# Kernel tuning notes

Hardware: AMD Instinct MI355X
Metric: run time of the kernel (lower is better)

## Reference

```python
import jax, jax.numpy as jnp
import numpy as np
from jax import lax

N, D, M, H = 8192, 32, 8, 128
ATOL = 1e-5
RTOL = 1e-5
MAX_STEPS = 10   # bounded adaptive dopri5 iterations (accept/reject with masking)
DT0 = 0.25


def setup_inputs() -> dict:
    key = jax.random.key(0)
    ks = jax.random.split(key, 6)
    p = lambda k, shape, s: jax.random.normal(k, shape, jnp.float32) * s
    return {
        "z": jax.random.normal(ks[0], (N, D), jnp.float32),
        "G_w": p(ks[1], (M, D), 0.3),
        "W1": p(ks[2], (H, D), (1.0 / D) ** 0.5),
        "b1": jnp.zeros((H,), jnp.float32),
        "W2": p(ks[3], (H, H), (1.0 / H) ** 0.5),
        "b2": jnp.zeros((H,), jnp.float32),
        "W3": p(ks[4], (D, H), (1.0 / H) ** 0.5),
        "b3": jnp.zeros((D,), jnp.float32),
        "T": jnp.ones((1,), jnp.float32),
    }


def qpnf_forward(z, G_w, W1, b1, W2, b2, W3, b3, T):
    d = z.shape[1]

    def mlp(x):  # dF network: d -> 128 -> 128 -> d
        h = jax.nn.relu(x @ W1.T + b1)
        h = jax.nn.relu(h @ W2.T + b2)
        return h @ W3.T + b3

    # G is linear (no bias) so jacrev(G)(x) == G_w for every sample; the batched
    # dG @ dG^T solves collapse to one shared (m,m) solve / (d,d) projector.
    A = G_w @ G_w.T                       # (m, m)
    AinvG = jnp.linalg.solve(A, G_w)      # (m, d) = A^{-1} W
    P = G_w.T @ AinvG                     # (d, d) null-space projector W^T A^{-1} W
    IP = jnp.eye(d, dtype=z.dtype) - P
    trP = jnp.trace(P)

    jac_mlp = jax.vmap(jax.jacrev(lambda xi: mlp(xi[None, :])[0]))  # (N,d,d)

    def f(y):  # augmented state y = [x | logp], dlogp/dt = -div(dx/dx)
        x = y[:, :d]
        dF = mlp(x)                        # (N, d)
        g = x @ G_w.T                      # (N, m)
        dz = -(dF @ IP) - g @ AinvG        # -(eta_J) - (eta_C)
        JdF = jac_mlp(x)                   # (N, d, d)
        # J_f = -(I-P) JdF - P  ->  dlogp = -trace(J_f)
        dlogp = jnp.einsum('jk,nkj->n', IP, JdF) + trP
        return jnp.concatenate([dz, dlogp[:, None]], axis=1)

    def rk_step(y, dt):  # Dormand-Prince 5(4)
        k1 = f(y)
        k2 = f(y + dt * (0.2 * k1))
        k3 = f(y + dt * (3/40 * k1 + 9/40 * k2))
        k4 = f(y + dt * (44/45 * k1 - 56/15 * k2 + 32/9 * k3))
        k5 = f(y + dt * (19372/6561 * k1 - 25360/2187 * k2 + 64448/6561 * k3 - 212/729 * k4))
        k6 = f(y + dt * (9017/3168 * k1 - 355/33 * k2 + 46732/5247 * k3 + 49/176 * k4 - 5103/18656 * k5))
        y1 = y + dt * (35/384 * k1 + 500/1113 * k3 + 125/192 * k4 - 2187/6784 * k5 + 11/84 * k6)
        k7 = f(y1)
        err = dt * ((35/384 - 5179/57600) * k1 + (500/1113 - 7571/16695) * k3
                    + (125/192 - 393/640) * k4 + (-2187/6784 + 92097/339200) * k5
                    + (11/84 - 187/2100) * k6 - (1/40) * k7)
        return y1, err

    t1 = 2.0 * T[0]  # eval path: integration_times[-1] *= 2
    y0 = jnp.concatenate([z, jnp.zeros((z.shape[0], 1), z.dtype)], axis=1)

    def body(carry, _):
        t, dt, y = carry
        done = t >= t1 - 1e-9
        dtc = jnp.where(done, jnp.asarray(1e-3, z.dtype), jnp.minimum(dt, t1 - t))
        y1, ev = rk_step(y, dtc)
        tol = ATOL + RTOL * jnp.maximum(jnp.abs(y), jnp.abs(y1))
        errn = jnp.sqrt(jnp.mean((ev / tol) ** 2))
        accept = jnp.logical_and(~done, errn <= 1.0)
        y_new = jnp.where(accept, y1, y)
        t_new = jnp.where(accept, t + dtc, t)
        factor = jnp.clip(0.9 * errn ** (-0.2), 0.2, 10.0)
        dt_new = jnp.where(done, dt, jnp.clip(dtc * factor, 1e-6, t1))
        dt_new = lax.stop_gradient(dt_new)
        return (t_new, dt_new, y_new), None

    init = (jnp.asarray(0.0, z.dtype), jnp.asarray(DT0, z.dtype), y0)
    (_, _, yT), _ = lax.scan(body, init, None, length=MAX_STEPS)
    return yT[:, :d]


def reference(z, G_w, W1, b1, W2, b2, W3, b3, T):
    return qpnf_forward(z, G_w, W1, b1, W2, b2, W3, b3, T)
```

## Files before the change

kernel.cpp:

```cpp
#include <hip/hip_runtime.h>
#include <hip/hip_cooperative_groups.h>
#include <math.h>

namespace cg = cooperative_groups;
typedef float4 f4;
typedef float2 f2;

#define NT 512
#define RB 32

#define WS_WR    0
#define WS_PART  32768
#define WS_TOTAL 35328

#define L_W1T   0
#define L_C3T   4096
#define L_PT    8320
#define L_XW    9472
#define L_H1W   10496
#define L_H2W   14592
#define L_KZ    18688
#define L_KL    26752
#define L_YZ    26976
#define L_Y1Z   28128
#define L_YL    29280
#define L_Y1L   29312
#define L_B1    29344
#define L_B2    29472
#define L_C0    29600
#define L_GS    29632
#define L_AAUG  29888
#define L_AINVG 30016
#define L_MISC  30272
#define LDS_FLOATS 30276
#define L_RED   L_H1W
#define L_P     L_H2W
#define L_IP    (L_H2W + 1024)
#define L_IPW3  L_KZ

__device__ const float ACO[5][5] = {
  { 0.2f, 0.f, 0.f, 0.f, 0.f },
  { (float)(3.0/40.0), (float)(9.0/40.0), 0.f, 0.f, 0.f },
  { (float)(44.0/45.0), (float)(-56.0/15.0), (float)(32.0/9.0), 0.f, 0.f },
  { (float)(19372.0/6561.0), (float)(-25360.0/2187.0), (float)(64448.0/6561.0), (float)(-212.0/729.0), 0.f },
  { (float)(9017.0/3168.0), (float)(-355.0/33.0), (float)(46732.0/5247.0), (float)(49.0/176.0), (float)(-5103.0/18656.0) }
};

#define B1C ((float)(35.0/384.0))
#define B3C ((float)(500.0/1113.0))
#define B4C ((float)(125.0/192.0))
#define B5C ((float)(-2187.0/6784.0))
#define B6C ((float)(11.0/84.0))

#define E1C ((float)(35.0/384.0 - 5179.0/57600.0))
#define E3C ((float)(500.0/1113.0 - 7571.0/16695.0))
#define E4C ((float)(125.0/192.0 - 393.0/640.0))
#define E5C ((float)(-2187.0/6784.0 + 92097.0/339200.0))
#define E6C ((float)(11.0/84.0 - 187.0/2100.0))
#define E7C ((float)(-1.0/40.0))

__device__ __forceinline__ f4 ld4(const float* p){ return *(const f4*)p; }
__device__ __forceinline__ void st4(float* p, f4 v){ *(f4*)p = v; }

__device__ __forceinline__ void assemble_x(float* lds, int tid, float dtc,
                                           const float* co, int np)
{
  const int w = tid >> 6, lane = tid & 63;
  const int r = lane >> 4;
  const int c = (lane << 1) & 31;
  const int o = (4 * w + r) * 36 + c;
  f2 y = *(const f2*)&lds[L_YZ + o];
  float sx = 0.f, sy = 0.f;
  for (int p = 0; p < np; p++){
    f2 kv = *(const f2*)&lds[L_KZ + p * 1152 + o];
    sx += co[p] * kv.x; sy += co[p] * kv.y;
  }
  float* XWp = &lds[L_XW + w * 128];
  XWp[(c + 0) * 4 + r] = y.x + dtc * sx;
  XWp[(c + 1) * 4 + r] = y.y + dtc * sy;
}

__device__ void eval_f(float* lds, const float* __restrict__ ws, int tid,
                       float trP, int kout)
{
  const int w = tid >> 6, lane = tid & 63;
  const int cg = lane & 31, kh = lane >> 5;
  float* XWp = &lds[L_XW  + w * 128];
  float* H1p = &lds[L_H1W + w * 512];
  float* H2p = &lds[L_H2W + w * 512];

  float a1[4][4];
#pragma unroll
  for (int i = 0; i < 4; i++)
#pragma unroll
    for (int j = 0; j < 4; j++) a1[i][j] = 0.f;
#pragma unroll 4
  for (int t = 0; t < 16; t++){
    const int k = kh * 16 + t;
    f4 xv = ld4(&XWp[k * 4]);
    f4 wv = ld4(&lds[L_W1T + k * 128 + 4 * cg]);
    const float* ap = (const float*)&xv;
    const float* bp = (const float*)&wv;
#pragma unroll
    for (int i = 0; i < 4; i++)
#pragma unroll
      for (int j = 0; j < 4; j++) a1[i][j] += bp[i] * ap[j];
  }
#pragma unroll
  for (int i = 0; i < 4; i++)
#pragma unroll
    for (int j = 0; j < 4; j++) a1[i][j] += __shfl_xor(a1[i][j], 32);
  if (kh == 0){
    f4 b1v = ld4(&lds[L_B1 + 4 * cg]);
    const float* b1p = (const float*)&b1v;
#pragma unroll
    for (int i = 0; i < 4; i++){
      f4 hv; float* hp = (float*)&hv;
#pragma unroll
      for (int j = 0; j < 4; j++) hp[j] = fmaxf(a1[i][j] + b1p[i], 0.f);
      st4(&H1p[(4 * cg + i) * 4], hv);
    }
  }
  __syncthreads();

  float ah[4][4], at[4][4];
#pragma unroll
  for (int i = 0; i < 4; i++)
#pragma unroll
    for (int j = 0; j < 4; j++){ ah[i][j] = 0.f; at[i][j] = 0.f; }
  const f4* WR4 = (const f4*)&ws[WS_WR];
  const int kb = kh * 64;
  f4 wb[4], rb[4];
#pragma unroll
  for (int u = 0; u < 4; u++){
    wb[u] = WR4[(kb + u) * 64 + cg];
    rb[u] = WR4[(kb + u) * 64 + 32 + cg];
  }
#pragma unroll 1
  for (int g = 0; g < 16; g++){
    f4 wc[4], rc[4];
#pragma unroll
    for (int u = 0; u < 4; u++){ wc[u] = wb[u]; rc[u] = rb[u]; }
    if (g < 15){
      const int kn = kb + (g + 1) * 4;
#pragma unroll
      for (int u = 0; u < 4; u++){
        wb[u] = WR4[(kn + u) * 64 + cg];
        rb[u] = WR4[(kn + u) * 64 + 32 + cg];
      }
    }
#pragma unroll
    for (int u = 0; u < 4; u++){
      const int k = kb + g * 4 + u;
      f4 av = ld4(&H1p[k * 4]);
      const float* ap = (const float*)&av;
      const float* wp = (const float*)&wc[u];
      const float* rp = (const float*)&rc[u];
      float m[4];
#pragma unroll
      for (int j = 0; j < 4; j++) m[j] = (ap[j] > 0.f) ? 1.f : 0.f;
#pragma unroll
      for (int i = 0; i < 4; i++)
#pragma unroll
        for (int j = 0; j < 4; j++){
          ah[i][j] += wp[i] * ap[j];
          at[i][j] += rp[i] * m[j];
        }
    }
  }
#pragma unroll
  for (int i = 0; i < 4; i++)
#pragma unroll
    for (int j = 0; j < 4; j++){
      ah[i][j] += __shfl_xor(ah[i][j], 32);
      at[i][j] += __shfl_xor(at[i][j], 32);
    }

  f4 b2v = ld4(&lds[L_B2 + 4 * cg]);
  const float* b2p = (const float*)&b2v;
  float h2v[4][4]; float dl[4] = {0.f, 0.f, 0.f, 0.f};
#pragma unroll
  for (int i = 0; i < 4; i++)
#pragma unroll
    for (int j = 0; j < 4; j++){
      float pre = ah[i][j] + b2p[i];
      float hv = fmaxf(pre, 0.f);
      h2v[i][j] = hv;
      if (pre > 0.f) dl[j] += at[i][j];
    }
#pragma unroll
  for (int mk = 1; mk < 32; mk <<= 1){
#pragma unroll
    for (int j = 0; j < 4; j++) dl[j] += __shfl_xor(dl[j], mk, 64);
  }
  if (kh == 0){
#pragma unroll
    for (int i = 0; i < 4; i++){
      f4 hv; float* hp = (float*)&hv;
#pragma unroll
      for (int j = 0; j < 4; j++) hp[j] = h2v[i][j];
      st4(&H2p[(4 * cg + i) * 4], hv);
    }
    if (cg == 0){
#pragma unroll
      for (int j = 0; j < 4; j++)
        lds[L_KL + kout * 32 + 4 * w + j] = dl[j] + trP;
    }
  }

  float a3[4] = {0.f, 0.f, 0.f, 0.f};
  const int bb = kh * 64;
#pragma unroll 4
  for (int t = 0; t < 16; t++){
    f4 cv = ld4(&lds[L_C3T + cg * 132 + bb + 4 * t]);
    const float* cp = (const float*)&cv;
#pragma unroll
    for (int u = 0; u < 4; u++){
      f4 av = ld4(&H2p[(bb + 4 * t + u) * 4]);
      const float* ap = (const float*)&av;
#pragma unroll
      for (int j = 0; j < 4; j++) a3[j] += ap[j] * cp[u];
    }
  }
  const int qq = kh * 16;
#pragma unroll
  for (int t = 0; t < 4; t++){
    f4 pv = ld4(&lds[L_PT + cg * 36 + qq + 4 * t]);
    const float* pp = (const float*)&pv;
#pragma unroll
    for (int u = 0; u < 4; u++){
      f4 av = ld4(&XWp[(qq + 4 * t + u) * 4]);
      const float* ap = (const float*)&av;
#pragma unroll
      for (int j = 0; j < 4; j++) a3[j] += ap[j] * pp[u];
    }
  }
#pragma unroll
  for (int j = 0; j < 4; j++) a3[j] += __shfl_xor(a3[j], 32);
  if (kh == 0){
    float c0v = lds[L_C0 + cg];
#pragma unroll
    for (int j = 0; j < 4; j++)
      lds[L_KZ + kout * 1152 + (4 * w + j) * 36 + cg] = -(a3[j] + c0v);
  }
}

__global__ void __launch_bounds__(NT, 2)
qpnf_kernel(const float* __restrict__ z, const float* __restrict__ Gw,
            const float* __restrict__ W1g, const float* __restrict__ b1g,
            const float* __restrict__ W2g, const float* __restrict__ b2g,
            const float* __restrict__ W3g, const float* __restrict__ b3g,
            const float* __restrict__ Tg, float* __restrict__ out,
            float* __restrict__ ws)
{
  __shared__ float lds[LDS_FLOATS];
  const int tid = threadIdx.x;
  const int bid = blockIdx.x;
  const int r0 = bid * RB;
  cg::grid_group grid = cg::this_grid();

  for (int i = 0; i < 8; i++){
    int idx = tid + i * NT;
    int h = idx >> 5, j = idx & 31;
    lds[L_W1T + j * 128 + h] = W1g[idx];
  }
  if (tid < 128){ lds[L_B1 + tid] = b1g[tid]; lds[L_B2 + tid] = b2g[tid]; }
  if (tid < 256) lds[L_GS + tid] = Gw[tid];
  __syncthreads();

  if (tid < 64){
    int i = tid >> 3, j = tid & 7;
    float s = 0.f;
    for (int k = 0; k < 32; k++) s += lds[L_GS + i * 32 + k] * lds[L_GS + j * 32 + k];
    lds[L_AAUG + i * 16 + j] = s;
    lds[L_AAUG + i * 16 + 8 + j] = (i == j) ? 1.f : 0.f;
  }
  __syncthreads();
  if (tid == 0){
    float* A = &lds[L_AAUG];
    for (int c = 0; c < 8; c++){
      int p = c; float mx = fabsf(A[c * 16 + c]);
      for (int r = c + 1; r < 8; r++){
        float v = fabsf(A[r * 16 + c]);
        if (v > mx){ mx = v; p = r; }
      }
      if (p != c)
        for (int q = 0; q < 16; q++){ float t = A[c*16+q]; A[c*16+q] = A[p*16+q]; A[p*16+q] = t; }
      float pv = 1.0f / A[c * 16 + c];
      for (int q = 0; q < 16; q++) A[c * 16 + q] *= pv;
      for (int r = 0; r < 8; r++) if (r != c){
        float fct = A[r * 16 + c];
        for (int q = 0; q < 16; q++) A[r * 16 + q] -= fct * A[c * 16 + q];
      }
    }
  }
  __syncthreads();
  if (tid < 256){
    int m = tid >> 5, d = tid & 31;
    float s = 0.f;
    for (int q = 0; q < 8; q++) s += lds[L_AAUG + m * 16 + 8 + q] * lds[L_GS + q * 32 + d];
    lds[L_AINVG + m * 32 + d] = s;
  }
  __syncthreads();
  for (int i4 = 0; i4 < 2; i4++){
    int idx = tid + i4 * NT;
    int i = idx >> 5, j = idx & 31;
    float s = 0.f;
    for (int m = 0; m < 8; m++) s += lds[L_GS + m * 32 + i] * lds[L_AINVG + m * 32 + j];
    lds[L_P + i * 32 + j] = s;
  }
  __syncthreads();
  float* IPl = &lds[L_IP];
  for (int i4 = 0; i4 < 2; i4++){
    int idx = tid + i4 * NT;
    int i = idx >> 5, j = idx & 31;
    IPl[i * 32 + j] = ((i == j) ? 1.f : 0.f) - lds[L_P + i * 32 + j];
  }
  if (tid == 0){
    float s = 0.f;
    for (int i = 0; i < 32; i++) s += lds[L_P + i * 32 + i];
    lds[L_MISC] = s;
  }
  __syncthreads();
  for (int i4 = 0; i4 < 8; i4++){
    int idx = tid + i4 * NT;
    int b = idx & 127, c = idx >> 7;
    float s = 0.f;
    for (int i = 0; i < 32; i++) s += W3g[i * 128 + b] * IPl[i * 32 + c];
    lds[L_C3T + c * 132 + b] = s;
  }
  for (int i4 = 0; i4 < 2; i4++){
    int idx = tid + i4 * NT;
    int c = idx >> 5, q = idx & 31;
    lds[L_PT + c * 36 + q] = lds[L_P + q * 32 + c];
  }
  if (tid < 32){
    float s = 0.f;
    for (int i = 0; i < 32; i++) s += b3g[i] * IPl[i * 32 + tid];
    lds[L_C0 + tid] = s;
  }
  for (int i4 = 0; i4 < 8; i4++){
    int idx = tid + i4 * NT;
    int j = idx >> 7, b = idx & 127;
    float s = 0.f;
    for (int k = 0; k < 32; k++) s += IPl[j * 32 + k] * W3g[k * 128 + b];
    lds[L_IPW3 + j * 128 + b] = s;
  }
  __syncthreads();
  if (bid < 128 && tid < 128){
    int a = bid;
    float s = 0.f;
    for (int j = 0; j < 32; j++) s += W1g[a * 32 + j] * lds[L_IPW3 + j * 128 + tid];
    ws[WS_WR + a * 256 + 128 + tid] = s * W2g[tid * 128 + a];
  }
  if (bid >= 128 && tid < 128){
    int a = bid - 128;
    ws[WS_WR + a * 256 + tid] = W2g[tid * 128 + a];
  }
  if (tid < 256){
    const int r = tid >> 3, jj = (tid & 7) * 4;
    st4(&lds[L_YZ + r * 36 + jj], ld4(&z[(r0 + r) * 32 + jj]));
  }
  if (tid < RB) lds[L_YL + tid] = 0.f;

  const float trP = lds[L_MISC];
  const float t1 = 2.0f * Tg[0];

  grid.sync();

  float t_cur = 0.f, dt_cur = 0.25f;
  bool prev_acc = false;

  for (int step = 0; step < 10; step++){
    if (t_cur >= t1 - 1e-9f) break;
    const float dtc = fminf(dt_cur, t1 - t_cur);

    for (int s = 1; s <= 6; s++){
      if (s == 1 && step > 0){
        if (prev_acc){
          const int w = tid >> 6, lane = tid & 63;
          const int r = lane >> 4, c = (lane << 1) & 31;
          const int o = (4 * w + r) * 36 + c;
          *(f2*)&lds[L_KZ + o] = *(const f2*)&lds[L_KZ + 6 * 1152 + o];
          if (lane < 4) lds[L_KL + 4 * w + lane] = lds[L_KL + 6 * 32 + 4 * w + lane];
        }
        continue;
      }
      assemble_x(lds, tid, dtc, ACO[s >= 2 ? s - 2 : 0], s - 1);
      eval_f(lds, ws, tid, trP, s - 1);
    }

    __syncthreads();
    if (tid < 256){
      const int r = tid >> 3, jj = (tid & 7) * 4;
      const int o = r * 36 + jj;
      f4 y   = ld4(&lds[L_YZ + o]);
      f4 k1v = ld4(&lds[L_KZ + 0 * 1152 + o]);
      f4 k3v = ld4(&lds[L_KZ + 2 * 1152 + o]);
      f4 k4v = ld4(&lds[L_KZ + 3 * 1152 + o]);
      f4 k5v = ld4(&lds[L_KZ + 4 * 1152 + o]);
      f4 k6v = ld4(&lds[L_KZ + 5 * 1152 + o]);
      f4 x;
      x.x = y.x + dtc * (B1C*k1v.x + B3C*k3v.x + B4C*k4v.x + B5C*k5v.x + B6C*k6v.x);
      x.y = y.y + dtc * (B1C*k1v.y + B3C*k3v.y + B4C*k4v.y + B5C*k5v.y + B6C*k6v.y);
      x.z = y.z + dtc * (B1C*k1v.z + B3C*k3v.z + B4C*k4v.z + B5C*k5v.z + B6C*k6v.z);
      x.w = y.w + dtc * (B1C*k1v.w + B3C*k3v.w + B4C*k4v.w + B5C*k5v.w + B6C*k6v.w);
      st4(&lds[L_Y1Z + o], x);
      float* XWp = &lds[L_XW + (r >> 2) * 128];
      const int rr = r & 3;
      XWp[(jj + 0) * 4 + rr] = x.x;
      XWp[(jj + 1) * 4 + rr] = x.y;
      XWp[(jj + 2) * 4 + rr] = x.z;
      XWp[(jj + 3) * 4 + rr] = x.w;
    }
    if (tid < RB){
      float s = B1C * lds[L_KL + 0*32 + tid] + B3C * lds[L_KL + 2*32 + tid]
              + B4C * lds[L_KL + 3*32 + tid] + B5C * lds[L_KL + 4*32 + tid]
              + B6C * lds[L_KL + 5*32 + tid];
      lds[L_Y1L + tid] = lds[L_YL + tid] + dtc * s;
    }
    __syncthreads();
    eval_f(lds, ws, tid, trP, 6);
    __syncthreads();

    float sacc = 0.f;
    if (tid < 256){
      const int r = tid >> 3, jj = (tid & 7) * 4;
      const int o = r * 36 + jj;
      f4 k1v = ld4(&lds[L_KZ + 0 * 1152 + o]);
      f4 k3v = ld4(&lds[L_KZ + 2 * 1152 + o]);
      f4 k4v = ld4(&lds[L_KZ + 3 * 1152 + o]);
      f4 k5v = ld4(&lds[L_KZ + 4 * 1152 + o]);
      f4 k6v = ld4(&lds[L_KZ + 5 * 1152 + o]);
      f4 k7v = ld4(&lds[L_KZ + 6 * 1152 + o]);
      f4 yv  = ld4(&lds[L_YZ + o]);
      f4 y1v = ld4(&lds[L_Y1Z + o]);
      float ev, tol, q;
      ev = dtc * (E1C*k1v.x + E3C*k3v.x + E4C*k4v.x + E5C*k5v.x + E6C*k6v.x + E7C*k7v.x);
      tol = 1e-5f + 1e-5f * fmaxf(fabsf(yv.x), fabsf(y1v.x)); q = ev / tol; sacc += q * q;
      ev = dtc * (E1C*k1v.y + E3C*k3v.y + E4C*k4v.y + E5C*k5v.y + E6C*k6v.y + E7C*k7v.y);
      tol = 1e-5f + 1e-5f * fmaxf(fabsf(yv.y), fabsf(y1v.y)); q = ev / tol; sacc += q * q;
      ev = dtc * (E1C*k1v.z + E3C*k3v.z + E4C*k4v.z + E5C*k5v.z + E6C*k6v.z + E7C*k7v.z);
      tol = 1e-5f + 1e-5f * fmaxf(fabsf(yv.z), fabsf(y1v.z)); q = ev / tol; sacc += q * q;
      ev = dtc * (E1C*k1v.w + E3C*k3v.w + E4C*k4v.w + E5C*k5v.w + E6C*k6v.w + E7C*k7v.w);
      tol = 1e-5f + 1e-5f * fmaxf(fabsf(yv.w), fabsf(y1v.w)); q = ev / tol; sacc += q * q;
    }
    if (tid < RB){
      float evl = dtc * (E1C * lds[L_KL + 0*32 + tid] + E3C * lds[L_KL + 2*32 + tid]
                + E4C * lds[L_KL + 3*32 + tid] + E5C * lds[L_KL + 4*32 + tid]
                + E6C * lds[L_KL + 5*32 + tid] + E7C * lds[L_KL + 6*32 + tid]);
      float toll = 1e-5f + 1e-5f * fmaxf(fabsf(lds[L_YL + tid]), fabsf(lds[L_Y1L + tid]));
      float ql = evl / toll; sacc += ql * ql;
    }
#pragma unroll
    for (int mk = 1; mk < 64; mk <<= 1) sacc += __shfl_xor(sacc, mk, 64);
    if ((tid & 63) == 0) lds[L_RED + (tid >> 6)] = sacc;
    __syncthreads();
    if (tid == 0){
      float s = lds[L_RED+0] + lds[L_RED+1] + lds[L_RED+2] + lds[L_RED+3]
              + lds[L_RED+4] + lds[L_RED+5] + lds[L_RED+6] + lds[L_RED+7];
      ws[WS_PART + step * 256 + bid] = s;
    }

    grid.sync();

    float ps = 0.f;
    if (tid < 256) ps = ws[WS_PART + step * 256 + tid];
#pragma unroll
    for (int mk = 1; mk < 64; mk <<= 1) ps += __shfl_xor(ps, mk, 64);
    if (tid < 256 && (tid & 63) == 0) lds[L_RED + (tid >> 6)] = ps;
    __syncthreads();
    const float errn = sqrtf((lds[L_RED+0] + lds[L_RED+1] + lds[L_RED+2] + lds[L_RED+3])
                             / 270336.0f);
    __syncthreads();

    const bool accept = (errn <= 1.0f);
    if (accept){
      const int w = tid >> 6, lane = tid & 63;
      const int r = lane >> 4, c = (lane << 1) & 31;
      const int o = (4 * w + r) * 36 + c;
      *(f2*)&lds[L_YZ + o] = *(const f2*)&lds[L_Y1Z + o];
      if (lane < 4) lds[L_YL + 4 * w + lane] = lds[L_Y1L + 4 * w + lane];
      t_cur += dtc;
    }
    float fac = 0.9f * powf(errn, -0.2f);
    fac = fminf(fmaxf(fac, 0.2f), 10.0f);
    dt_cur = fminf(fmaxf(dtc * fac, 1e-6f), t1);
    prev_acc = accept;
  }

  __syncthreads();
  if (tid < 256){
    const int r = tid >> 3, jj = (tid & 7) * 4;
    st4(&out[(r0 + r) * 32 + jj], ld4(&lds[L_YZ + r * 36 + jj]));
  }
}

extern "C" void kernel_launch(void* const* d_in, const int* in_sizes, int n_in,
                              void* d_out, int out_size, void* d_ws, size_t ws_size,
                              hipStream_t stream)
{
  (void)in_sizes; (void)n_in; (void)out_size;
  const float* z  = (const float*)d_in[0];
  const float* Gw = (const float*)d_in[1];
  const float* W1 = (const float*)d_in[2];
  const float* b1 = (const float*)d_in[3];
  const float* W2 = (const float*)d_in[4];
  const float* b2 = (const float*)d_in[5];
  const float* W3 = (const float*)d_in[6];
  const float* b3 = (const float*)d_in[7];
  const float* T  = (const float*)d_in[8];
  float* out = (float*)d_out;
  float* ws  = (float*)d_ws;
  if (ws_size < (size_t)WS_TOTAL * sizeof(float)) return;

  void* args[] = { (void*)&z, (void*)&Gw, (void*)&W1, (void*)&b1, (void*)&W2,
                   (void*)&b2, (void*)&W3, (void*)&b3, (void*)&T, (void*)&out,
                   (void*)&ws };
  hipLaunchCooperativeKernel((const void*)qpnf_kernel, dim3(256), dim3(NT),
                             args, 0, stream);
}
```

Baseline: 1.189 ms.

## Pair warps on two row groups in layer-2 GEMM to halve weight global loads

The layer-2 GEMM (h and Jacobian-trace accumulators) is restructured so each pair of wavefronts shares two 4-row groups and splits the K dimension, with each thread accumulating 8 columns instead of 4. Each wave now streams half as much of the W2/R weight data from global memory per row. Partial sums from the second wave go through a new LDS scratch area, which costs extra syncthreads and LDS. Launch bounds drop to one block per SM to allow the doubled accumulator register count, which reduces occupancy.

```diff
diff --git a/kernel.cpp b/kernel.cpp
--- a/kernel.cpp
+++ b/kernel.cpp
@@ -32,7 +32,8 @@
 #define L_AAUG  29888
 #define L_AINVG 30016
 #define L_MISC  30272
-#define LDS_FLOATS 30276
+#define L_S     30276
+#define LDS_FLOATS (30276 + 4*32*68)
 #define L_RED   L_H1W
 #define L_P     L_H2W
 #define L_IP    (L_H2W + 1024)
@@ -85,9 +86,22 @@
 {
   const int w = tid >> 6, lane = tid & 63;
   const int cg = lane & 31, kh = lane >> 5;
+  const int p  = w >> 1;
+  const int kg = w & 1;
   float* XWp = &lds[L_XW  + w * 128];
   float* H1p = &lds[L_H1W + w * 512];
-  float* H2p = &lds[L_H2W + w * 512];
+  float* H1e = &lds[L_H1W + (2 * p) * 512];
+  float* H1o = &lds[L_H1W + (2 * p + 1) * 512];
+  float* H2w = &lds[L_H2W + w * 512];
+
+  const f4* WR4 = (const f4*)&ws[WS_WR];
+  const int kb = kg * 64 + kh * 32;
+  f4 wb[4], rb[4];
+#pragma unroll
+  for (int u = 0; u < 4; u++){
+    wb[u] = WR4[(kb + u) * 64 + cg];
+    rb[u] = WR4[(kb + u) * 64 + 32 + cg];
+  }
 
   float a1[4][4];
 #pragma unroll
@@ -123,25 +137,17 @@
   }
   __syncthreads();
 
-  float ah[4][4], at[4][4];
+  float ah[4][8], at[4][8];
 #pragma unroll
   for (int i = 0; i < 4; i++)
 #pragma unroll
-    for (int j = 0; j < 4; j++){ ah[i][j] = 0.f; at[i][j] = 0.f; }
-  const f4* WR4 = (const f4*)&ws[WS_WR];
-  const int kb = kh * 64;
-  f4 wb[4], rb[4];
-#pragma unroll
-  for (int u = 0; u < 4; u++){
-    wb[u] = WR4[(kb + u) * 64 + cg];
-    rb[u] = WR4[(kb + u) * 64 + 32 + cg];
-  }
+    for (int j = 0; j < 8; j++){ ah[i][j] = 0.f; at[i][j] = 0.f; }
 #pragma unroll 1
-  for (int g = 0; g < 16; g++){
+  for (int g = 0; g < 8; g++){
     f4 wc[4], rc[4];
 #pragma unroll
     for (int u = 0; u < 4; u++){ wc[u] = wb[u]; rc[u] = rb[u]; }
-    if (g < 15){
+    if (g < 7){
       const int kn = kb + (g + 1) * 4;
 #pragma unroll
       for (int u = 0; u < 4; u++){
@@ -152,61 +158,105 @@
 #pragma unroll
     for (int u = 0; u < 4; u++){
       const int k = kb + g * 4 + u;
-      f4 av = ld4(&H1p[k * 4]);
-      const float* ap = (const float*)&av;
+      f4 ae = ld4(&H1e[k * 4]);
+      f4 ao = ld4(&H1o[k * 4]);
+      const float* aep = (const float*)&ae;
+      const float* aop = (const float*)&ao;
       const float* wp = (const float*)&wc[u];
       const float* rp = (const float*)&rc[u];
-      float m[4];
-#pragma unroll
-      for (int j = 0; j < 4; j++) m[j] = (ap[j] > 0.f) ? 1.f : 0.f;
-#pragma unroll
-      for (int i = 0; i < 4; i++)
+      float me[4], mo[4];
+#pragma unroll
+      for (int j = 0; j < 4; j++){
+        me[j] = (aep[j] > 0.f) ? 1.f : 0.f;
+        mo[j] = (aop[j] > 0.f) ? 1.f : 0.f;
+      }
+#pragma unroll
+      for (int i = 0; i < 4; i++){
 #pragma unroll
         for (int j = 0; j < 4; j++){
-          ah[i][j] += wp[i] * ap[j];
-          at[i][j] += rp[i] * m[j];
+          ah[i][j]     += wp[i] * aep[j];
+          at[i][j]     += rp[i] * me[j];
+          ah[i][4 + j] += wp[i] * aop[j];
+          at[i][4 + j] += rp[i] * mo[j];
         }
+      }
     }
   }
 #pragma unroll
   for (int i = 0; i < 4; i++)
 #pragma unroll
-    for (int j = 0; j < 4; j++){
+    for (int j = 0; j < 8; j++){
       ah[i][j] += __shfl_xor(ah[i][j], 32);
       at[i][j] += __shfl_xor(at[i][j], 32);
     }
 
-  f4 b2v = ld4(&lds[L_B2 + 4 * cg]);
-  const float* b2p = (const float*)&b2v;
-  float h2v[4][4]; float dl[4] = {0.f, 0.f, 0.f, 0.f};
-#pragma unroll
-  for (int i = 0; i < 4; i++)
-#pragma unroll
-    for (int j = 0; j < 4; j++){
-      float pre = ah[i][j] + b2p[i];
-      float hv = fmaxf(pre, 0.f);
-      h2v[i][j] = hv;
-      if (pre > 0.f) dl[j] += at[i][j];
-    }
-#pragma unroll
-  for (int mk = 1; mk < 32; mk <<= 1){
-#pragma unroll
-    for (int j = 0; j < 4; j++) dl[j] += __shfl_xor(dl[j], mk, 64);
-  }
-  if (kh == 0){
+  float* S = &lds[L_S + (p * 32 + cg) * 68];
+  if (kg == 1 && kh == 0){
 #pragma unroll
     for (int i = 0; i < 4; i++){
-      f4 hv; float* hp = (float*)&hv;
-#pragma unroll
-      for (int j = 0; j < 4; j++) hp[j] = h2v[i][j];
-      st4(&H2p[(4 * cg + i) * 4], hv);
-    }
-    if (cg == 0){
-#pragma unroll
-      for (int j = 0; j < 4; j++)
-        lds[L_KL + kout * 32 + 4 * w + j] = dl[j] + trP;
-    }
-  }
+      f4 a, b; float* apx = (float*)&a; float* bpx = (float*)&b;
+#pragma unroll
+      for (int j = 0; j < 4; j++){ apx[j] = ah[i][j]; bpx[j] = ah[i][4 + j]; }
+      st4(&S[i * 8], a); st4(&S[i * 8 + 4], b);
+#pragma unroll
+      for (int j = 0; j < 4; j++){ apx[j] = at[i][j]; bpx[j] = at[i][4 + j]; }
+      st4(&S[32 + i * 8], a); st4(&S[32 + i * 8 + 4], b);
+    }
+  }
+  __syncthreads();
+
+  if (kg == 0){
+#pragma unroll
+    for (int i = 0; i < 4; i++){
+      f4 a = ld4(&S[i * 8]), b = ld4(&S[i * 8 + 4]);
+      const float* apx = (const float*)&a; const float* bpx = (const float*)&b;
+#pragma unroll
+      for (int j = 0; j < 4; j++){ ah[i][j] += apx[j]; ah[i][4 + j] += bpx[j]; }
+      a = ld4(&S[32 + i * 8]); b = ld4(&S[32 + i * 8 + 4]);
+      apx = (const float*)&a; bpx = (const float*)&b;
+#pragma unroll
+      for (int j = 0; j < 4; j++){ at[i][j] += apx[j]; at[i][4 + j] += bpx[j]; }
+    }
+    f4 b2v = ld4(&lds[L_B2 + 4 * cg]);
+    const float* b2p = (const float*)&b2v;
+    float h2v[4][8]; float dl[8] = {0.f,0.f,0.f,0.f,0.f,0.f,0.f,0.f};
+#pragma unroll
+    for (int i = 0; i < 4; i++)
+#pragma unroll
+      for (int j = 0; j < 8; j++){
+        float pre = ah[i][j] + b2p[i];
+        float hv = fmaxf(pre, 0.f);
+        h2v[i][j] = hv;
+        if (pre > 0.f) dl[j] += at[i][j];
+      }
+    if (kh){
+#pragma unroll
+      for (int j = 0; j < 8; j++) dl[j] = 0.f;
+    }
+#pragma unroll
+    for (int mk = 1; mk < 64; mk <<= 1){
+#pragma unroll
+      for (int j = 0; j < 8; j++) dl[j] += __shfl_xor(dl[j], mk, 64);
+    }
+    if (kh == 0){
+      float* H2e = &lds[L_H2W + (2 * p) * 512];
+      float* H2o = &lds[L_H2W + (2 * p + 1) * 512];
+#pragma unroll
+      for (int i = 0; i < 4; i++){
+        f4 a, b; float* apx = (float*)&a; float* bpx = (float*)&b;
+#pragma unroll
+        for (int j = 0; j < 4; j++){ apx[j] = h2v[i][j]; bpx[j] = h2v[i][4 + j]; }
+        st4(&H2e[(4 * cg + i) * 4], a);
+        st4(&H2o[(4 * cg + i) * 4], b);
+      }
+    }
+    if (lane == 0){
+#pragma unroll
+      for (int j = 0; j < 8; j++)
+        lds[L_KL + kout * 32 + 8 * p + j] = dl[j] + trP;
+    }
+  }
+  __syncthreads();
 
   float a3[4] = {0.f, 0.f, 0.f, 0.f};
   const int bb = kh * 64;
@@ -216,7 +266,7 @@
     const float* cp = (const float*)&cv;
 #pragma unroll
     for (int u = 0; u < 4; u++){
-      f4 av = ld4(&H2p[(bb + 4 * t + u) * 4]);
+      f4 av = ld4(&H2w[(bb + 4 * t + u) * 4]);
       const float* ap = (const float*)&av;
 #pragma unroll
       for (int j = 0; j < 4; j++) a3[j] += ap[j] * cp[u];
@@ -245,7 +295,7 @@
   }
 }
 
-__global__ void __launch_bounds__(NT, 2)
+__global__ void __launch_bounds__(NT, 1)
 qpnf_kernel(const float* __restrict__ z, const float* __restrict__ Gw,
             const float* __restrict__ W1g, const float* __restrict__ b1g,
             const float* __restrict__ W2g, const float* __restrict__ b2g,
```

After: 1.454 ms. 22.3% more time.

## Double block size to 1024 threads and split per-row MLP work across two waves

Applied to the files above, without the earlier changes.

Raises the block to 1024 threads (16 waves) and splits each 4-row group's MLP evaluation between two waves. Each wave handles 2 rows in layer 1 and layer 3, and half of the hidden outputs in layer 2. The layer-2 divergence partial sums are combined through a new LDS slot, which needs an extra barrier. This is meant to raise occupancy and latency hiding per CU, at the cost of more barriers, smaller per-thread register tiles, and losing the register double-buffered prefetch of the global weights. Launch bounds change to (1024,4) and the setup loops are adapted to the new thread count.

```diff
diff --git a/kernel.cpp b/kernel.cpp
--- a/kernel.cpp
+++ b/kernel.cpp
@@ -6,7 +6,7 @@
 typedef float4 f4;
 typedef float2 f2;
 
-#define NT 512
+#define NT 1024
 #define RB 32
 
 #define WS_WR    0
@@ -32,7 +32,8 @@
 #define L_AAUG  29888
 #define L_AINVG 30016
 #define L_MISC  30272
-#define LDS_FLOATS 30276
+#define L_DL    30276
+#define LDS_FLOATS 30340
 #define L_RED   L_H1W
 #define L_P     L_H2W
 #define L_IP    (L_H2W + 1024)
@@ -66,186 +67,165 @@
                                            const float* co, int np)
 {
   const int w = tid >> 6, lane = tid & 63;
-  const int r = lane >> 4;
-  const int c = (lane << 1) & 31;
-  const int o = (4 * w + r) * 36 + c;
-  f2 y = *(const f2*)&lds[L_YZ + o];
-  float sx = 0.f, sy = 0.f;
-  for (int p = 0; p < np; p++){
-    f2 kv = *(const f2*)&lds[L_KZ + p * 1152 + o];
-    sx += co[p] * kv.x; sy += co[p] * kv.y;
-  }
-  float* XWp = &lds[L_XW + w * 128];
-  XWp[(c + 0) * 4 + r] = y.x + dtc * sx;
-  XWp[(c + 1) * 4 + r] = y.y + dtc * sy;
+  const int g = w & 7, hi = w >> 3;
+  const int rr = lane >> 5, c = lane & 31;
+  const int o = (4 * g + 2 * hi + rr) * 36 + c;
+  float y = lds[L_YZ + o];
+  float s = 0.f;
+  for (int p = 0; p < np; p++) s += co[p] * lds[L_KZ + p * 1152 + o];
+  lds[L_XW + g * 128 + c * 4 + 2 * hi + rr] = y + dtc * s;
 }
 
 __device__ void eval_f(float* lds, const float* __restrict__ ws, int tid,
                        float trP, int kout)
 {
   const int w = tid >> 6, lane = tid & 63;
-  const int cg = lane & 31, kh = lane >> 5;
-  float* XWp = &lds[L_XW  + w * 128];
-  float* H1p = &lds[L_H1W + w * 512];
-  float* H2p = &lds[L_H2W + w * 512];
-
-  float a1[4][4];
+  const int g = w & 7, hi = w >> 3;
+  float* XWp = &lds[L_XW + g * 128];
+  float* H1p = &lds[L_H1W + g * 512];
+  float* H2p = &lds[L_H2W + g * 512];
+
+  {
+    const int cg = lane & 31, kh = lane >> 5;
+    float a1[4][2];
+#pragma unroll
+    for (int i = 0; i < 4; i++){ a1[i][0] = 0.f; a1[i][1] = 0.f; }
+#pragma unroll 4
+    for (int t = 0; t < 16; t++){
+      const int k = kh * 16 + t;
+      f2 xv = *(const f2*)&XWp[k * 4 + 2 * hi];
+      f4 wv = ld4(&lds[L_W1T + k * 128 + 4 * cg]);
+      const float* wp = (const float*)&wv;
+#pragma unroll
+      for (int i = 0; i < 4; i++){
+        a1[i][0] += wp[i] * xv.x;
+        a1[i][1] += wp[i] * xv.y;
+      }
+    }
+#pragma unroll
+    for (int i = 0; i < 4; i++){
+      a1[i][0] += __shfl_xor(a1[i][0], 32);
+      a1[i][1] += __shfl_xor(a1[i][1], 32);
+    }
+    if (kh == 0){
+      f4 b1v = ld4(&lds[L_B1 + 4 * cg]);
+      const float* b1p = (const float*)&b1v;
+#pragma unroll
+      for (int i = 0; i < 4; i++){
+        f2 hv;
+        hv.x = fmaxf(a1[i][0] + b1p[i], 0.f);
+        hv.y = fmaxf(a1[i][1] + b1p[i], 0.f);
+        *(f2*)&H1p[(4 * cg + i) * 4 + 2 * hi] = hv;
+      }
+    }
+  }
+  __syncthreads();
+
+  const int ccg = lane & 15, kq = lane >> 4;
+  float ah[4][4], at[4][4];
 #pragma unroll
   for (int i = 0; i < 4; i++)
 #pragma unroll
-    for (int j = 0; j < 4; j++) a1[i][j] = 0.f;
+    for (int j = 0; j < 4; j++){ ah[i][j] = 0.f; at[i][j] = 0.f; }
+  const f4* WR4 = (const f4*)&ws[WS_WR];
 #pragma unroll 4
-  for (int t = 0; t < 16; t++){
-    const int k = kh * 16 + t;
-    f4 xv = ld4(&XWp[k * 4]);
-    f4 wv = ld4(&lds[L_W1T + k * 128 + 4 * cg]);
-    const float* ap = (const float*)&xv;
-    const float* bp = (const float*)&wv;
+  for (int t = 0; t < 32; t++){
+    const int k = 4 * t + kq;
+    f4 wv = WR4[k * 64 + 16 * hi + ccg];
+    f4 rv = WR4[k * 64 + 32 + 16 * hi + ccg];
+    f4 av = ld4(&H1p[k * 4]);
+    const float* wp = (const float*)&wv;
+    const float* rp = (const float*)&rv;
+    const float* ap = (const float*)&av;
+    float m[4];
+#pragma unroll
+    for (int j = 0; j < 4; j++) m[j] = (ap[j] > 0.f) ? 1.f : 0.f;
 #pragma unroll
     for (int i = 0; i < 4; i++)
 #pragma unroll
-      for (int j = 0; j < 4; j++) a1[i][j] += bp[i] * ap[j];
+      for (int j = 0; j < 4; j++){
+        ah[i][j] += wp[i] * ap[j];
+        at[i][j] += rp[i] * m[j];
+      }
   }
 #pragma unroll
   for (int i = 0; i < 4; i++)
 #pragma unroll
-    for (int j = 0; j < 4; j++) a1[i][j] += __shfl_xor(a1[i][j], 32);
-  if (kh == 0){
-    f4 b1v = ld4(&lds[L_B1 + 4 * cg]);
-    const float* b1p = (const float*)&b1v;
+    for (int j = 0; j < 4; j++){
+      ah[i][j] += __shfl_xor(ah[i][j], 16);
+      ah[i][j] += __shfl_xor(ah[i][j], 32);
+      at[i][j] += __shfl_xor(at[i][j], 16);
+      at[i][j] += __shfl_xor(at[i][j], 32);
+    }
+  float dl[4] = {0.f, 0.f, 0.f, 0.f};
+  if (kq == 0){
+    f4 b2v = ld4(&lds[L_B2 + 64 * hi + 4 * ccg]);
+    const float* b2p = (const float*)&b2v;
 #pragma unroll
     for (int i = 0; i < 4; i++){
       f4 hv; float* hp = (float*)&hv;
 #pragma unroll
-      for (int j = 0; j < 4; j++) hp[j] = fmaxf(a1[i][j] + b1p[i], 0.f);
-      st4(&H1p[(4 * cg + i) * 4], hv);
-    }
-  }
-  __syncthreads();
-
-  float ah[4][4], at[4][4];
-#pragma unroll
-  for (int i = 0; i < 4; i++)
-#pragma unroll
-    for (int j = 0; j < 4; j++){ ah[i][j] = 0.f; at[i][j] = 0.f; }
-  const f4* WR4 = (const f4*)&ws[WS_WR];
-  const int kb = kh * 64;
-  f4 wb[4], rb[4];
-#pragma unroll
-  for (int u = 0; u < 4; u++){
-    wb[u] = WR4[(kb + u) * 64 + cg];
-    rb[u] = WR4[(kb + u) * 64 + 32 + cg];
-  }
-#pragma unroll 1
-  for (int g = 0; g < 16; g++){
-    f4 wc[4], rc[4];
-#pragma unroll
-    for (int u = 0; u < 4; u++){ wc[u] = wb[u]; rc[u] = rb[u]; }
-    if (g < 15){
-      const int kn = kb + (g + 1) * 4;
+      for (int j = 0; j < 4; j++){
+        float pre = ah[i][j] + b2p[i];
+        hp[j] = fmaxf(pre, 0.f);
+        if (pre > 0.f) dl[j] += at[i][j];
+      }
+      st4(&H2p[(64 * hi + 4 * ccg + i) * 4], hv);
+    }
+  }
+#pragma unroll
+  for (int mk = 1; mk < 16; mk <<= 1){
+#pragma unroll
+    for (int j = 0; j < 4; j++) dl[j] += __shfl_xor(dl[j], mk);
+  }
+  if (lane == 0){
+#pragma unroll
+    for (int j = 0; j < 4; j++) lds[L_DL + g * 8 + hi * 4 + j] = dl[j];
+  }
+  __syncthreads();
+
+  if (hi == 0 && lane < 4)
+    lds[L_KL + kout * 32 + 4 * g + lane] =
+        lds[L_DL + g * 8 + lane] + lds[L_DL + g * 8 + 4 + lane] + trP;
+
+  {
+    const int c3 = lane & 31, bh = lane >> 5;
+    float a30 = 0.f, a31 = 0.f;
+    const int bb = bh * 64;
+#pragma unroll 4
+    for (int t = 0; t < 16; t++){
+      f4 cv = ld4(&lds[L_C3T + c3 * 132 + bb + 4 * t]);
+      const float* cp = (const float*)&cv;
 #pragma unroll
       for (int u = 0; u < 4; u++){
-        wb[u] = WR4[(kn + u) * 64 + cg];
-        rb[u] = WR4[(kn + u) * 64 + 32 + cg];
-      }
-    }
-#pragma unroll
-    for (int u = 0; u < 4; u++){
-      const int k = kb + g * 4 + u;
-      f4 av = ld4(&H1p[k * 4]);
-      const float* ap = (const float*)&av;
-      const float* wp = (const float*)&wc[u];
-      const float* rp = (const float*)&rc[u];
-      float m[4];
-#pragma unroll
-      for (int j = 0; j < 4; j++) m[j] = (ap[j] > 0.f) ? 1.f : 0.f;
-#pragma unroll
-      for (int i = 0; i < 4; i++)
-#pragma unroll
-        for (int j = 0; j < 4; j++){
-          ah[i][j] += wp[i] * ap[j];
-          at[i][j] += rp[i] * m[j];
-        }
-    }
-  }
-#pragma unroll
-  for (int i = 0; i < 4; i++)
-#pragma unroll
-    for (int j = 0; j < 4; j++){
-      ah[i][j] += __shfl_xor(ah[i][j], 32);
-      at[i][j] += __shfl_xor(at[i][j], 32);
-    }
-
-  f4 b2v = ld4(&lds[L_B2 + 4 * cg]);
-  const float* b2p = (const float*)&b2v;
-  float h2v[4][4]; float dl[4] = {0.f, 0.f, 0.f, 0.f};
-#pragma unroll
-  for (int i = 0; i < 4; i++)
-#pragma unroll
-    for (int j = 0; j < 4; j++){
-      float pre = ah[i][j] + b2p[i];
-      float hv = fmaxf(pre, 0.f);
-      h2v[i][j] = hv;
-      if (pre > 0.f) dl[j] += at[i][j];
-    }
-#pragma unroll
-  for (int mk = 1; mk < 32; mk <<= 1){
-#pragma unroll
-    for (int j = 0; j < 4; j++) dl[j] += __shfl_xor(dl[j], mk, 64);
-  }
-  if (kh == 0){
-#pragma unroll
-    for (int i = 0; i < 4; i++){
-      f4 hv; float* hp = (float*)&hv;
-#pragma unroll
-      for (int j = 0; j < 4; j++) hp[j] = h2v[i][j];
-      st4(&H2p[(4 * cg + i) * 4], hv);
-    }
-    if (cg == 0){
-#pragma unroll
-      for (int j = 0; j < 4; j++)
-        lds[L_KL + kout * 32 + 4 * w + j] = dl[j] + trP;
-    }
-  }
-
-  float a3[4] = {0.f, 0.f, 0.f, 0.f};
-  const int bb = kh * 64;
-#pragma unroll 4
-  for (int t = 0; t < 16; t++){
-    f4 cv = ld4(&lds[L_C3T + cg * 132 + bb + 4 * t]);
-    const float* cp = (const float*)&cv;
-#pragma unroll
-    for (int u = 0; u < 4; u++){
-      f4 av = ld4(&H2p[(bb + 4 * t + u) * 4]);
-      const float* ap = (const float*)&av;
-#pragma unroll
-      for (int j = 0; j < 4; j++) a3[j] += ap[j] * cp[u];
-    }
-  }
-  const int qq = kh * 16;
-#pragma unroll
-  for (int t = 0; t < 4; t++){
-    f4 pv = ld4(&lds[L_PT + cg * 36 + qq + 4 * t]);
-    const float* pp = (const float*)&pv;
-#pragma unroll
-    for (int u = 0; u < 4; u++){
-      f4 av = ld4(&XWp[(qq + 4 * t + u) * 4]);
-      const float* ap = (const float*)&av;
-#pragma unroll
-      for (int j = 0; j < 4; j++) a3[j] += ap[j] * pp[u];
-    }
-  }
-#pragma unroll
-  for (int j = 0; j < 4; j++) a3[j] += __shfl_xor(a3[j], 32);
-  if (kh == 0){
-    float c0v = lds[L_C0 + cg];
-#pragma unroll
-    for (int j = 0; j < 4; j++)
-      lds[L_KZ + kout * 1152 + (4 * w + j) * 36 + cg] = -(a3[j] + c0v);
+        f2 av = *(const f2*)&H2p[(bb + 4 * t + u) * 4 + 2 * hi];
+        a30 += av.x * cp[u];
+        a31 += av.y * cp[u];
+      }
+    }
+    const int qq = bh * 16;
+#pragma unroll
+    for (int t = 0; t < 4; t++){
+      f4 pv = ld4(&lds[L_PT + c3 * 36 + qq + 4 * t]);
+      const float* pp = (const float*)&pv;
+#pragma unroll
+      for (int u = 0; u < 4; u++){
+        f2 xv = *(const f2*)&XWp[(qq + 4 * t + u) * 4 + 2 * hi];
+        a30 += xv.x * pp[u];
+        a31 += xv.y * pp[u];
+      }
+    }
+    a30 += __shfl_xor(a30, 32);
+    a31 += __shfl_xor(a31, 32);
+    if (bh == 0){
+      float c0v = lds[L_C0 + c3];
+      lds[L_KZ + kout * 1152 + (4 * g + 2 * hi + 0) * 36 + c3] = -(a30 + c0v);
+      lds[L_KZ + kout * 1152 + (4 * g + 2 * hi + 1) * 36 + c3] = -(a31 + c0v);
+    }
   }
 }
 
-__global__ void __launch_bounds__(NT, 2)
+__global__ void __launch_bounds__(NT, 4)
 qpnf_kernel(const float* __restrict__ z, const float* __restrict__ Gw,
             const float* __restrict__ W1g, const float* __restrict__ b1g,
             const float* __restrict__ W2g, const float* __restrict__ b2g,
@@ -259,8 +239,7 @@
   const int r0 = bid * RB;
   cg::grid_group grid = cg::this_grid();
 
-  for (int i = 0; i < 8; i++){
-    int idx = tid + i * NT;
+  for (int idx = tid; idx < 4096; idx += NT){
     int h = idx >> 5, j = idx & 31;
     lds[L_W1T + j * 128 + h] = W1g[idx];
   }
@@ -302,18 +281,16 @@
     lds[L_AINVG + m * 32 + d] = s;
   }
   __syncthreads();
-  for (int i4 = 0; i4 < 2; i4++){
-    int idx = tid + i4 * NT;
-    int i = idx >> 5, j = idx & 31;
+  {
+    int i = tid >> 5, j = tid & 31;
     float s = 0.f;
     for (int m = 0; m < 8; m++) s += lds[L_GS + m * 32 + i] * lds[L_AINVG + m * 32 + j];
     lds[L_P + i * 32 + j] = s;
   }
   __syncthreads();
   float* IPl = &lds[L_IP];
-  for (int i4 = 0; i4 < 2; i4++){
-    int idx = tid + i4 * NT;
-    int i = idx >> 5, j = idx & 31;
+  {
+    int i = tid >> 5, j = tid & 31;
     IPl[i * 32 + j] = ((i == j) ? 1.f : 0.f) - lds[L_P + i * 32 + j];
   }
   if (tid == 0){
@@ -322,16 +299,14 @@
     lds[L_MISC] = s;
   }
   __syncthreads();
-  for (int i4 = 0; i4 < 8; i4++){
-    int idx = tid + i4 * NT;
+  for (int idx = tid; idx < 4096; idx += NT){
     int b = idx & 127, c = idx >> 7;
     float s = 0.f;
     for (int i = 0; i < 32; i++) s += W3g[i * 128 + b] * IPl[i * 32 + c];
     lds[L_C3T + c * 132 + b] = s;
   }
-  for (int i4 = 0; i4 < 2; i4++){
-    int idx = tid + i4 * NT;
-    int c = idx >> 5, q = idx & 31;
+  {
+    int c = tid >> 5, q = tid & 31;
     lds[L_PT + c * 36 + q] = lds[L_P + q * 32 + c];
   }
   if (tid < 32){
@@ -339,8 +314,7 @@
     for (int i = 0; i < 32; i++) s += b3g[i] * IPl[i * 32 + tid];
     lds[L_C0 + tid] = s;
   }
-  for (int i4 = 0; i4 < 8; i4++){
-    int idx = tid + i4 * NT;
+  for (int idx = tid; idx < 4096; idx += NT){
     int j = idx >> 7, b = idx & 127;
     float s = 0.f;
     for (int k = 0; k < 32; k++) s += IPl[j * 32 + k] * W3g[k * 128 + b];
@@ -378,12 +352,14 @@
     for (int s = 1; s <= 6; s++){
       if (s == 1 && step > 0){
         if (prev_acc){
-          const int w = tid >> 6, lane = tid & 63;
-          const int r = lane >> 4, c = (lane << 1) & 31;
-          const int o = (4 * w + r) * 36 + c;
-          *(f2*)&lds[L_KZ + o] = *(const f2*)&lds[L_KZ + 6 * 1152 + o];
-          if (lane < 4) lds[L_KL + 4 * w + lane] = lds[L_KL + 6 * 32 + 4 * w + lane];
+          if (tid < 256){
+            const int r = tid >> 3, jj = (tid & 7) * 4;
+            const int o = r * 36 + jj;
+            st4(&lds[L_KZ + o], ld4(&lds[L_KZ + 6 * 1152 + o]));
+          }
+          if (tid < RB) lds[L_KL + tid] = lds[L_KL + 6 * 32 + tid];
         }
+        __syncthreads();
         continue;
       }
       assemble_x(lds, tid, dtc, ACO[s >= 2 ? s - 2 : 0], s - 1);
@@ -457,8 +433,8 @@
     if ((tid & 63) == 0) lds[L_RED + (tid >> 6)] = sacc;
     __syncthreads();
     if (tid == 0){
-      float s = lds[L_RED+0] + lds[L_RED+1] + lds[L_RED+2] + lds[L_RED+3]
-              + lds[L_RED+4] + lds[L_RED+5] + lds[L_RED+6] + lds[L_RED+7];
+      float s = 0.f;
+      for (int i = 0; i < 16; i++) s += lds[L_RED + i];
       ws[WS_PART + step * 256 + bid] = s;
     }
 
@@ -476,11 +452,12 @@
 
     const bool accept = (errn <= 1.0f);
     if (accept){
-      const int w = tid >> 6, lane = tid & 63;
-      const int r = lane >> 4, c = (lane << 1) & 31;
-      const int o = (4 * w + r) * 36 + c;
-      *(f2*)&lds[L_YZ + o] = *(const f2*)&lds[L_Y1Z + o];
-      if (lane < 4) lds[L_YL + 4 * w + lane] = lds[L_Y1L + 4 * w + lane];
+      if (tid < 256){
+        const int r = tid >> 3, jj = (tid & 7) * 4;
+        const int o = r * 36 + jj;
+        st4(&lds[L_YZ + o], ld4(&lds[L_Y1Z + o]));
+      }
+      if (tid < RB) lds[L_YL + tid] = lds[L_Y1L + tid];
       t_cur += dtc;
     }
     float fac = 0.9f * powf(errn, -0.2f);
```

New measurement: 1.391 ms. 17.0% more time.
